# Optimization experiments

Hardware: AMD Instinct MI355X
Metric: run time of the kernel (lower is better)

The kernel has to match this reference:

```python
import jax, jax.numpy as jnp
import numpy as np

GROUPS = 32
EPS = 1e-6


def group_norm(x, gamma, beta):
    b, c, h, w = x.shape
    xg = x.reshape(b, GROUPS, c // GROUPS, h, w)
    mu = xg.mean(axis=(2, 3, 4), keepdims=True)
    var = xg.var(axis=(2, 3, 4), keepdims=True)
    xn = ((xg - mu) * jax.lax.rsqrt(var + EPS)).reshape(b, c, h, w)
    return xn * gamma[None, :, None, None] + beta[None, :, None, None]


def conv1x1(x, w, b):
    # x: (b,c_in,h,w), w: (c_out,c_in), b: (c_out,)
    return jnp.einsum('oc,bchw->bohw', w, x) + b[None, :, None, None]


def setup_inputs() -> dict:
    key = jax.random.key(0)
    ks = jax.random.split(key, 10)
    c = 512
    scale = 1.0 / np.sqrt(c)
    inp = jax.random.normal(ks[0], (16, c, 32, 32), dtype=jnp.float32)
    return {
        'inp': inp,
        'gamma': jnp.ones((c,), jnp.float32),
        'beta': jnp.zeros((c,), jnp.float32),
        'Wq': jax.random.normal(ks[1], (c, c), jnp.float32) * scale,
        'bq': jnp.zeros((c,), jnp.float32),
        'Wk': jax.random.normal(ks[2], (c, c), jnp.float32) * scale,
        'bk': jnp.zeros((c,), jnp.float32),
        'Wv': jax.random.normal(ks[3], (c, c), jnp.float32) * scale,
        'bv': jnp.zeros((c,), jnp.float32),
        'Wo': jax.random.normal(ks[4], (c, c), jnp.float32) * scale,
        'bo': jnp.zeros((c,), jnp.float32),
    }


def reference(inp, gamma, beta, Wq, bq, Wk, bk, Wv, bv, Wo, bo):
    b, c, h, w = inp.shape
    x = group_norm(inp, gamma, beta)
    Q = conv1x1(x, Wq, bq).reshape(b, c, h * w)  # (b,c,n)
    K = conv1x1(x, Wk, bk).reshape(b, c, h * w)  # (b,c,m)
    V = conv1x1(x, Wv, bv).reshape(b, c, h * w)  # (b,c,m)
    # attn[b,n,m] = sum_c Q[b,c,n] * K[b,c,m], scaled then softmax over m
    attn = jnp.einsum('bcn,bcm->bnm', Q, K) / jnp.sqrt(jnp.float32(c))
    attn = jax.nn.softmax(attn, axis=2)
    # A[b,c,n] = sum_m V[b,c,m] * attn[b,n,m]  (== bmm(V, attn^T))
    A = jnp.einsum('bcm,bnm->bcn', V, attn).reshape(b, c, h, w)
    A = conv1x1(A, Wo, bo)
    return inp + A
```

## Files before the change

kernel.cpp:

```cpp
#include <hip/hip_runtime.h>

typedef unsigned short UST;
typedef __attribute__((ext_vector_type(8))) short bf16x8;
typedef __attribute__((ext_vector_type(4))) float f32x4;

__device__ __forceinline__ UST f2bf(float f) {
  union { float f; unsigned int u; } x; x.f = f;
  unsigned int r = x.u + 0x7fffu + ((x.u >> 16) & 1u);
  return (UST)(r >> 16);
}

typedef const __attribute__((address_space(1))) unsigned int* gptr32;
typedef __attribute__((address_space(3))) unsigned int* lptr32;

__device__ __forceinline__ void load16(const void* g, void* l) {
  __builtin_amdgcn_global_load_lds((gptr32)(unsigned long long)g,
                                   (lptr32)(unsigned int)(unsigned long long)l,
                                   16, 0, 0);
}

__global__ __launch_bounds__(256) void conv_w(
    const float4* __restrict__ a, const float4* __restrict__ b,
    const float4* __restrict__ c, const float4* __restrict__ d,
    ushort4* __restrict__ oa, ushort4* __restrict__ ob,
    ushort4* __restrict__ oc, ushort4* __restrict__ od) {
  int i = blockIdx.x * 256 + threadIdx.x;
  float4 v;
  v = a[i]; oa[i] = make_ushort4(f2bf(v.x), f2bf(v.y), f2bf(v.z), f2bf(v.w));
  v = b[i]; ob[i] = make_ushort4(f2bf(v.x), f2bf(v.y), f2bf(v.z), f2bf(v.w));
  v = c[i]; oc[i] = make_ushort4(f2bf(v.x), f2bf(v.y), f2bf(v.z), f2bf(v.w));
  v = d[i]; od[i] = make_ushort4(f2bf(v.x), f2bf(v.y), f2bf(v.z), f2bf(v.w));
}

__global__ __launch_bounds__(256) void gn_stats(const float* __restrict__ inp,
                                                float* __restrict__ stats) {
  const int bg = blockIdx.x;
  const int tid = threadIdx.x;
  const float4* p = (const float4*)(inp + (size_t)bg * 16384);
  float s = 0.f, ss = 0.f;
#pragma unroll
  for (int i = 0; i < 16; i++) {
    float4 t = p[tid + i * 256];
    s += t.x + t.y + t.z + t.w;
    ss += t.x * t.x + t.y * t.y + t.z * t.z + t.w * t.w;
  }
  for (int o = 32; o >= 1; o >>= 1) { s += __shfl_xor(s, o); ss += __shfl_xor(ss, o); }
  __shared__ float red[8];
  const int w = tid >> 6;
  if ((tid & 63) == 0) { red[w * 2] = s; red[w * 2 + 1] = ss; }
  __syncthreads();
  if (tid == 0) {
    float S1 = red[0] + red[2] + red[4] + red[6];
    float S2 = red[1] + red[3] + red[5] + red[7];
    float mu = S1 * (1.f / 16384.f);
    float var = S2 * (1.f / 16384.f) - mu * mu;
    stats[bg * 2] = mu;
    stats[bg * 2 + 1] = rsqrtf(var + 1e-6f);
  }
}

__global__ __launch_bounds__(64) void gn_apply(
    const float* __restrict__ inp, const float* __restrict__ gamma,
    const float* __restrict__ beta, const float* __restrict__ stats,
    UST* __restrict__ Xnt) {
  const int lane = threadIdx.x;
  const int nc = blockIdx.x, g = blockIdx.y, b = blockIdx.z;
  const float mu = stats[(b * 32 + g) * 2];
  const float rstd = stats[(b * 32 + g) * 2 + 1];
  const int n = nc * 64 + lane;
  UST o[16];
#pragma unroll
  for (int j = 0; j < 16; j++) {
    int c = g * 16 + j;
    float sc = gamma[c] * rstd;
    float sh = beta[c] - mu * sc;
    float x = inp[((size_t)b * 512 + c) * 1024 + n];
    o[j] = f2bf(x * sc + sh);
  }
  UST* dst = Xnt + ((size_t)b * 1024 + n) * 512 + g * 16;
#pragma unroll
  for (int q = 0; q < 4; q++)
    ((ushort4*)dst)[q] = make_ushort4(o[q * 4], o[q * 4 + 1], o[q * 4 + 2], o[q * 4 + 3]);
}

__global__ __launch_bounds__(256) void softmax_k(const float* __restrict__ S,
                                                 UST* __restrict__ P) {
  const int w = threadIdx.x >> 6, lane = threadIdx.x & 63;
  const size_t row = (size_t)blockIdx.x * 4 + w;
  const float4* Sr = (const float4*)(S + row * 1024);
  float v[16];
#pragma unroll
  for (int j = 0; j < 4; j++) {
    float4 t = Sr[j * 64 + lane];
    v[j * 4 + 0] = t.x; v[j * 4 + 1] = t.y; v[j * 4 + 2] = t.z; v[j * 4 + 3] = t.w;
  }
  float m = v[0];
#pragma unroll
  for (int i = 1; i < 16; i++) m = fmaxf(m, v[i]);
#pragma unroll
  for (int o = 32; o >= 1; o >>= 1) m = fmaxf(m, __shfl_xor(m, o));
  float s = 0.f;
#pragma unroll
  for (int i = 0; i < 16; i++) { v[i] = __expf(v[i] - m); s += v[i]; }
#pragma unroll
  for (int o = 32; o >= 1; o >>= 1) s += __shfl_xor(s, o);
  const float rs = 1.f / s;
  ushort4* Pr = (ushort4*)(P + row * 1024);
#pragma unroll
  for (int j = 0; j < 4; j++)
    Pr[j * 64 + lane] = make_ushort4(f2bf(v[j * 4] * rs), f2bf(v[j * 4 + 1] * rs),
                                     f2bf(v[j * 4 + 2] * rs), f2bf(v[j * 4 + 3] * rs));
}

template <int EPI>
__global__ __launch_bounds__(256, 2) void gemm_bt(
    const UST* __restrict__ A, const UST* __restrict__ B, void* __restrict__ C,
    const float* __restrict__ bias, const float* __restrict__ extra, float scale,
    int M, int N, int K, long strideA, long strideB, long strideC) {
  __shared__ __align__(16) UST lA[128 * 32];
  __shared__ __align__(16) UST lB[128 * 32];

  const int tid = threadIdx.x;
  const int z = blockIdx.z;
  const int m0 = blockIdx.y * 128;
  const int n0 = blockIdx.x * 128;
  const UST* Ab = A + (long)z * strideA;
  const UST* Bb = B + (long)z * strideB;

  const int w = tid >> 6, lane = tid & 63;
  const int quad = lane >> 4, l16 = lane & 15;
  const int wm = w >> 1, wn = w & 1;

  f32x4 acc[4][4];
#pragma unroll
  for (int i = 0; i < 4; i++)
#pragma unroll
    for (int j = 0; j < 4; j++) acc[i][j] = f32x4{0.f, 0.f, 0.f, 0.f};

  const int rowa = tid >> 2;
  const int kc = (tid & 3) * 8;
  const UST* gA = Ab + (size_t)(m0 + rowa) * K + kc;
  const UST* gB = Bb + (size_t)(n0 + rowa) * K + kc;
  char* lAw = (char*)lA + (w << 10);
  char* lBw = (char*)lB + (w << 10);

  for (int k0 = 0; k0 < K; k0 += 32) {
    __syncthreads();
    load16(gA, lAw);
    load16(gA + (size_t)64 * K, lAw + 4096);
    load16(gB, lBw);
    load16(gB + (size_t)64 * K, lBw + 4096);
    gA += 32; gB += 32;
    __syncthreads();
    bf16x8 af[4], bfr[4];
#pragma unroll
    for (int i = 0; i < 4; i++)
      af[i] = *(const bf16x8*)(lA + (wm * 64 + i * 16 + l16) * 32 + quad * 8);
#pragma unroll
    for (int j = 0; j < 4; j++)
      bfr[j] = *(const bf16x8*)(lB + (wn * 64 + j * 16 + l16) * 32 + quad * 8);
#pragma unroll
    for (int i = 0; i < 4; i++)
#pragma unroll
      for (int j = 0; j < 4; j++)
        acc[i][j] = __builtin_amdgcn_mfma_f32_16x16x32_bf16(af[i], bfr[j], acc[i][j], 0, 0, 0);
  }

  const int gr0 = m0 + wm * 64 + quad * 4;
  const int gc0 = n0 + wn * 64 + l16;
  if constexpr (EPI == 2 || EPI == 4) {
    float* Cb = (float*)C + (long)z * strideC;
#pragma unroll
    for (int i = 0; i < 4; i++)
#pragma unroll
      for (int j = 0; j < 4; j++) {
        const int gc = gc0 + j * 16;
#pragma unroll
        for (int r = 0; r < 4; r++) {
          const int gr = gr0 + i * 16 + r;
          float v = acc[i][j][r];
          if constexpr (EPI == 2) v *= scale;
          if constexpr (EPI == 4) v += bias[gr] + extra[(long)z * strideC + (size_t)gr * N + gc];
          Cb[(size_t)gr * N + gc] = v;
        }
      }
  } else {
    UST* Cb = (UST*)C + (long)z * strideC;
#pragma unroll
    for (int i = 0; i < 4; i++)
#pragma unroll
      for (int j = 0; j < 4; j++) {
        const int gc = gc0 + j * 16;
        float bc = 0.f;
        if constexpr (EPI == 0) bc = bias[gc];
#pragma unroll
        for (int r = 0; r < 4; r++) {
          const int gr = gr0 + i * 16 + r;
          float v = acc[i][j][r] + bc;
          if constexpr (EPI == 1) v += bias[gr];
          Cb[(size_t)gr * N + gc] = f2bf(v);
        }
      }
  }
}

extern "C" void kernel_launch(void* const* d_in, const int* in_sizes, int n_in,
                              void* d_out, int out_size, void* d_ws, size_t ws_size,
                              hipStream_t stream) {
  const float* inp   = (const float*)d_in[0];
  const float* gamma = (const float*)d_in[1];
  const float* beta  = (const float*)d_in[2];
  const float* Wq    = (const float*)d_in[3];
  const float* bq    = (const float*)d_in[4];
  const float* Wk    = (const float*)d_in[5];
  const float* bk    = (const float*)d_in[6];
  const float* Wv    = (const float*)d_in[7];
  const float* bv    = (const float*)d_in[8];
  const float* Wo    = (const float*)d_in[9];
  const float* bo    = (const float*)d_in[10];
  float* out = (float*)d_out;
  char* ws = (char*)d_ws;

  UST*   Xnt   = (UST*)(ws);
  UST*   Qt    = (UST*)(ws + ((size_t)16 << 20));
  UST*   Kt    = (UST*)(ws + ((size_t)32 << 20));
  UST*   V     = (UST*)(ws + ((size_t)48 << 20));
  float* S     = (float*)(ws + ((size_t)64 << 20));
  float* stats = (float*)(ws + ((size_t)128 << 20));
  UST*   Wqb   = (UST*)(ws + ((size_t)128 << 20) + 8192);
  UST*   Wkb   = Wqb + 262144;
  UST*   Wvb   = Wkb + 262144;
  UST*   Wob   = Wvb + 262144;
  UST*   P     = Qt;
  UST*   At    = Xnt;

  conv_w<<<256, 256, 0, stream>>>((const float4*)Wq, (const float4*)Wk,
                                  (const float4*)Wv, (const float4*)Wo,
                                  (ushort4*)Wqb, (ushort4*)Wkb, (ushort4*)Wvb, (ushort4*)Wob);
  gn_stats<<<512, 256, 0, stream>>>(inp, stats);
  gn_apply<<<dim3(16, 32, 16), 64, 0, stream>>>(inp, gamma, beta, stats, Xnt);

  gemm_bt<0><<<dim3(4, 128, 1), 256, 0, stream>>>(Xnt, Wqb, Qt, bq, nullptr, 1.f,
                                                  16384, 512, 512, 0, 0, 0);
  gemm_bt<0><<<dim3(4, 128, 1), 256, 0, stream>>>(Xnt, Wkb, Kt, bk, nullptr, 1.f,
                                                  16384, 512, 512, 0, 0, 0);
  gemm_bt<1><<<dim3(8, 4, 16), 256, 0, stream>>>(Wvb, Xnt, V, bv, nullptr, 1.f,
                                                 512, 1024, 512, 0, 524288, 524288);
  gemm_bt<2><<<dim3(8, 8, 16), 256, 0, stream>>>(Qt, Kt, S, nullptr, nullptr,
                                                 0.04419417382415922f,
                                                 1024, 1024, 512, 524288, 524288, 1048576);
  softmax_k<<<4096, 256, 0, stream>>>(S, P);
  gemm_bt<3><<<dim3(4, 8, 16), 256, 0, stream>>>(P, V, At, nullptr, nullptr, 1.f,
                                                 1024, 512, 1024, 1048576, 524288, 524288);
  gemm_bt<4><<<dim3(8, 4, 16), 256, 0, stream>>>(Wob, At, out, bo, inp, 1.f,
                                                 512, 1024, 512, 0, 524288, 524288);
}
```

Measured before the change: 262.4 us.

## Fuse groupnorm passes, merge Q/K projections, store scores in bf16, blocked layout

Result: faster. 245.1 us (-6.6%).

```diff
diff --git a/kernel.cpp b/kernel.cpp
--- a/kernel.cpp
+++ b/kernel.cpp
@@ -2,6 +2,7 @@
 
 typedef unsigned short UST;
 typedef __attribute__((ext_vector_type(8))) short bf16x8;
+typedef __attribute__((ext_vector_type(8))) unsigned short us8;
 typedef __attribute__((ext_vector_type(4))) float f32x4;
 
 __device__ __forceinline__ UST f2bf(float f) {
@@ -9,6 +10,10 @@
   unsigned int r = x.u + 0x7fffu + ((x.u >> 16) & 1u);
   return (UST)(r >> 16);
 }
+__device__ __forceinline__ float bf2f(UST h) {
+  union { unsigned int u; float f; } x; x.u = ((unsigned int)h) << 16;
+  return x.f;
+}
 
 typedef const __attribute__((address_space(1))) unsigned int* gptr32;
 typedef __attribute__((address_space(3))) unsigned int* lptr32;
@@ -23,29 +28,38 @@
     const float4* __restrict__ a, const float4* __restrict__ b,
     const float4* __restrict__ c, const float4* __restrict__ d,
     ushort4* __restrict__ oa, ushort4* __restrict__ ob,
-    ushort4* __restrict__ oc, ushort4* __restrict__ od) {
+    ushort4* __restrict__ oc, ushort4* __restrict__ od,
+    const float4* __restrict__ bq4, const float4* __restrict__ bk4,
+    float4* __restrict__ bqk4) {
   int i = blockIdx.x * 256 + threadIdx.x;
   float4 v;
   v = a[i]; oa[i] = make_ushort4(f2bf(v.x), f2bf(v.y), f2bf(v.z), f2bf(v.w));
   v = b[i]; ob[i] = make_ushort4(f2bf(v.x), f2bf(v.y), f2bf(v.z), f2bf(v.w));
   v = c[i]; oc[i] = make_ushort4(f2bf(v.x), f2bf(v.y), f2bf(v.z), f2bf(v.w));
   v = d[i]; od[i] = make_ushort4(f2bf(v.x), f2bf(v.y), f2bf(v.z), f2bf(v.w));
-}
-
-__global__ __launch_bounds__(256) void gn_stats(const float* __restrict__ inp,
-                                                float* __restrict__ stats) {
-  const int bg = blockIdx.x;
+  if (blockIdx.x == 0) {
+    int t = threadIdx.x;
+    bqk4[t] = (t < 128) ? bq4[t] : bk4[t - 128];
+  }
+}
+
+__global__ __launch_bounds__(256) void gn_fused(
+    const float* __restrict__ inp, const float* __restrict__ gamma,
+    const float* __restrict__ beta, UST* __restrict__ Xnt) {
+  const int g = blockIdx.x & 31, b = blockIdx.x >> 5;
   const int tid = threadIdx.x;
-  const float4* p = (const float4*)(inp + (size_t)bg * 16384);
+  const float* base = inp + ((size_t)b * 32 + g) * 16384;
+  const float4* p4 = (const float4*)base;
   float s = 0.f, ss = 0.f;
 #pragma unroll
   for (int i = 0; i < 16; i++) {
-    float4 t = p[tid + i * 256];
+    float4 t = p4[tid + i * 256];
     s += t.x + t.y + t.z + t.w;
     ss += t.x * t.x + t.y * t.y + t.z * t.z + t.w * t.w;
   }
   for (int o = 32; o >= 1; o >>= 1) { s += __shfl_xor(s, o); ss += __shfl_xor(ss, o); }
   __shared__ float red[8];
+  __shared__ float mu_s, rstd_s;
   const int w = tid >> 6;
   if ((tid & 63) == 0) { red[w * 2] = s; red[w * 2 + 1] = ss; }
   __syncthreads();
@@ -54,46 +68,43 @@
     float S2 = red[1] + red[3] + red[5] + red[7];
     float mu = S1 * (1.f / 16384.f);
     float var = S2 * (1.f / 16384.f) - mu * mu;
-    stats[bg * 2] = mu;
-    stats[bg * 2 + 1] = rsqrtf(var + 1e-6f);
-  }
-}
-
-__global__ __launch_bounds__(64) void gn_apply(
-    const float* __restrict__ inp, const float* __restrict__ gamma,
-    const float* __restrict__ beta, const float* __restrict__ stats,
-    UST* __restrict__ Xnt) {
-  const int lane = threadIdx.x;
-  const int nc = blockIdx.x, g = blockIdx.y, b = blockIdx.z;
-  const float mu = stats[(b * 32 + g) * 2];
-  const float rstd = stats[(b * 32 + g) * 2 + 1];
-  const int n = nc * 64 + lane;
-  UST o[16];
-#pragma unroll
-  for (int j = 0; j < 16; j++) {
-    int c = g * 16 + j;
-    float sc = gamma[c] * rstd;
-    float sh = beta[c] - mu * sc;
-    float x = inp[((size_t)b * 512 + c) * 1024 + n];
-    o[j] = f2bf(x * sc + sh);
-  }
-  UST* dst = Xnt + ((size_t)b * 1024 + n) * 512 + g * 16;
-#pragma unroll
-  for (int q = 0; q < 4; q++)
-    ((ushort4*)dst)[q] = make_ushort4(o[q * 4], o[q * 4 + 1], o[q * 4 + 2], o[q * 4 + 3]);
-}
-
-__global__ __launch_bounds__(256) void softmax_k(const float* __restrict__ S,
+    mu_s = mu; rstd_s = rsqrtf(var + 1e-6f);
+  }
+  __syncthreads();
+  const float mu = mu_s, rstd = rstd_s;
+#pragma unroll
+  for (int cc = 0; cc < 2; cc++) {
+    const int ccg = g * 2 + cc;
+    float sc[8], sh[8];
+#pragma unroll
+    for (int j = 0; j < 8; j++) {
+      int ch = ccg * 8 + j;
+      sc[j] = gamma[ch] * rstd;
+      sh[j] = beta[ch] - mu * sc[j];
+    }
+#pragma unroll
+    for (int i = 0; i < 4; i++) {
+      const int n = tid + i * 256;
+      us8 v;
+#pragma unroll
+      for (int j = 0; j < 8; j++) {
+        float x = inp[((size_t)b * 512 + ccg * 8 + j) * 1024 + n];
+        v[j] = f2bf(x * sc[j] + sh[j]);
+      }
+      *(us8*)(Xnt + (size_t)b * 524288 + (size_t)ccg * 8192 + (size_t)n * 8) = v;
+    }
+  }
+}
+
+__global__ __launch_bounds__(256) void softmax_k(const UST* __restrict__ S,
                                                  UST* __restrict__ P) {
   const int w = threadIdx.x >> 6, lane = threadIdx.x & 63;
   const size_t row = (size_t)blockIdx.x * 4 + w;
-  const float4* Sr = (const float4*)(S + row * 1024);
+  const us8* Sr = (const us8*)(S + row * 1024);
+  us8 a = Sr[lane], b = Sr[64 + lane];
   float v[16];
 #pragma unroll
-  for (int j = 0; j < 4; j++) {
-    float4 t = Sr[j * 64 + lane];
-    v[j * 4 + 0] = t.x; v[j * 4 + 1] = t.y; v[j * 4 + 2] = t.z; v[j * 4 + 3] = t.w;
-  }
+  for (int j = 0; j < 8; j++) { v[j] = bf2f(a[j]); v[8 + j] = bf2f(b[j]); }
   float m = v[0];
 #pragma unroll
   for (int i = 1; i < 16; i++) m = fmaxf(m, v[i]);
@@ -105,18 +116,20 @@
 #pragma unroll
   for (int o = 32; o >= 1; o >>= 1) s += __shfl_xor(s, o);
   const float rs = 1.f / s;
-  ushort4* Pr = (ushort4*)(P + row * 1024);
-#pragma unroll
-  for (int j = 0; j < 4; j++)
-    Pr[j * 64 + lane] = make_ushort4(f2bf(v[j * 4] * rs), f2bf(v[j * 4 + 1] * rs),
-                                     f2bf(v[j * 4 + 2] * rs), f2bf(v[j * 4 + 3] * rs));
+  us8* Pr = (us8*)(P + row * 1024);
+  us8 oa, ob;
+#pragma unroll
+  for (int j = 0; j < 8; j++) { oa[j] = f2bf(v[j] * rs); ob[j] = f2bf(v[8 + j] * rs); }
+  Pr[lane] = oa; Pr[64 + lane] = ob;
 }
 
 template <int EPI>
 __global__ __launch_bounds__(256, 2) void gemm_bt(
     const UST* __restrict__ A, const UST* __restrict__ B, void* __restrict__ C,
     const float* __restrict__ bias, const float* __restrict__ extra, float scale,
-    int M, int N, int K, long strideA, long strideB, long strideC) {
+    int N, int K, int ldc,
+    int rsA, int csA, int ssA, int rsB, int csB, int ssB,
+    long zA, long zB, long zC) {
   __shared__ __align__(16) UST lA[128 * 32];
   __shared__ __align__(16) UST lB[128 * 32];
 
@@ -124,8 +137,8 @@
   const int z = blockIdx.z;
   const int m0 = blockIdx.y * 128;
   const int n0 = blockIdx.x * 128;
-  const UST* Ab = A + (long)z * strideA;
-  const UST* Bb = B + (long)z * strideB;
+  const UST* Ab = A + (long)z * zA;
+  const UST* Bb = B + (long)z * zB;
 
   const int w = tid >> 6, lane = tid & 63;
   const int quad = lane >> 4, l16 = lane & 15;
@@ -138,19 +151,19 @@
     for (int j = 0; j < 4; j++) acc[i][j] = f32x4{0.f, 0.f, 0.f, 0.f};
 
   const int rowa = tid >> 2;
-  const int kc = (tid & 3) * 8;
-  const UST* gA = Ab + (size_t)(m0 + rowa) * K + kc;
-  const UST* gB = Bb + (size_t)(n0 + rowa) * K + kc;
+  const int kchunk = tid & 3;
+  const UST* gA = Ab + (size_t)(m0 + rowa) * rsA + (size_t)kchunk * csA;
+  const UST* gB = Bb + (size_t)(n0 + rowa) * rsB + (size_t)kchunk * csB;
   char* lAw = (char*)lA + (w << 10);
   char* lBw = (char*)lB + (w << 10);
 
   for (int k0 = 0; k0 < K; k0 += 32) {
     __syncthreads();
     load16(gA, lAw);
-    load16(gA + (size_t)64 * K, lAw + 4096);
+    load16(gA + (size_t)64 * rsA, lAw + 4096);
     load16(gB, lBw);
-    load16(gB + (size_t)64 * K, lBw + 4096);
-    gA += 32; gB += 32;
+    load16(gB + (size_t)64 * rsB, lBw + 4096);
+    gA += ssA; gB += ssB;
     __syncthreads();
     bf16x8 af[4], bfr[4];
 #pragma unroll
@@ -168,8 +181,8 @@
 
   const int gr0 = m0 + wm * 64 + quad * 4;
   const int gc0 = n0 + wn * 64 + l16;
-  if constexpr (EPI == 2 || EPI == 4) {
-    float* Cb = (float*)C + (long)z * strideC;
+  if constexpr (EPI == 4) {
+    float* Cb = (float*)C + (long)z * zC;
 #pragma unroll
     for (int i = 0; i < 4; i++)
 #pragma unroll
@@ -178,14 +191,12 @@
 #pragma unroll
         for (int r = 0; r < 4; r++) {
           const int gr = gr0 + i * 16 + r;
-          float v = acc[i][j][r];
-          if constexpr (EPI == 2) v *= scale;
-          if constexpr (EPI == 4) v += bias[gr] + extra[(long)z * strideC + (size_t)gr * N + gc];
-          Cb[(size_t)gr * N + gc] = v;
+          float v = acc[i][j][r] + bias[gr] + extra[(long)z * zC + (size_t)gr * ldc + gc];
+          Cb[(size_t)gr * ldc + gc] = v;
         }
       }
   } else {
-    UST* Cb = (UST*)C + (long)z * strideC;
+    UST* Cb = (UST*)C + (long)z * zC;
 #pragma unroll
     for (int i = 0; i < 4; i++)
 #pragma unroll
@@ -198,7 +209,8 @@
           const int gr = gr0 + i * 16 + r;
           float v = acc[i][j][r] + bc;
           if constexpr (EPI == 1) v += bias[gr];
-          Cb[(size_t)gr * N + gc] = f2bf(v);
+          if constexpr (EPI == 5) v *= scale;
+          Cb[(size_t)gr * ldc + gc] = f2bf(v);
         }
       }
   }
@@ -221,37 +233,37 @@
   float* out = (float*)d_out;
   char* ws = (char*)d_ws;
 
-  UST*   Xnt   = (UST*)(ws);
-  UST*   Qt    = (UST*)(ws + ((size_t)16 << 20));
-  UST*   Kt    = (UST*)(ws + ((size_t)32 << 20));
-  UST*   V     = (UST*)(ws + ((size_t)48 << 20));
-  float* S     = (float*)(ws + ((size_t)64 << 20));
-  float* stats = (float*)(ws + ((size_t)128 << 20));
-  UST*   Wqb   = (UST*)(ws + ((size_t)128 << 20) + 8192);
-  UST*   Wkb   = Wqb + 262144;
-  UST*   Wvb   = Wkb + 262144;
-  UST*   Wob   = Wvb + 262144;
-  UST*   P     = Qt;
-  UST*   At    = Xnt;
-
-  conv_w<<<256, 256, 0, stream>>>((const float4*)Wq, (const float4*)Wk,
-                                  (const float4*)Wv, (const float4*)Wo,
-                                  (ushort4*)Wqb, (ushort4*)Wkb, (ushort4*)Wvb, (ushort4*)Wob);
-  gn_stats<<<512, 256, 0, stream>>>(inp, stats);
-  gn_apply<<<dim3(16, 32, 16), 64, 0, stream>>>(inp, gamma, beta, stats, Xnt);
-
-  gemm_bt<0><<<dim3(4, 128, 1), 256, 0, stream>>>(Xnt, Wqb, Qt, bq, nullptr, 1.f,
-                                                  16384, 512, 512, 0, 0, 0);
-  gemm_bt<0><<<dim3(4, 128, 1), 256, 0, stream>>>(Xnt, Wkb, Kt, bk, nullptr, 1.f,
-                                                  16384, 512, 512, 0, 0, 0);
-  gemm_bt<1><<<dim3(8, 4, 16), 256, 0, stream>>>(Wvb, Xnt, V, bv, nullptr, 1.f,
-                                                 512, 1024, 512, 0, 524288, 524288);
-  gemm_bt<2><<<dim3(8, 8, 16), 256, 0, stream>>>(Qt, Kt, S, nullptr, nullptr,
-                                                 0.04419417382415922f,
-                                                 1024, 1024, 512, 524288, 524288, 1048576);
+  UST*   Xnt  = (UST*)(ws);
+  UST*   QKt  = (UST*)(ws + ((size_t)16 << 20));
+  UST*   V    = (UST*)(ws + ((size_t)48 << 20));
+  UST*   S    = (UST*)(ws + ((size_t)64 << 20));
+  float* bqk  = (float*)(ws + ((size_t)96 << 20));
+  UST*   Wqkb = (UST*)(ws + ((size_t)96 << 20) + 8192);
+  UST*   Wvb  = Wqkb + 524288;
+  UST*   Wob  = Wvb + 262144;
+  UST*   P    = QKt;
+  UST*   At   = Xnt;
+
+  conv_w<<<256, 256, 0, stream>>>(
+      (const float4*)Wq, (const float4*)Wk, (const float4*)Wv, (const float4*)Wo,
+      (ushort4*)Wqkb, (ushort4*)(Wqkb + 262144), (ushort4*)Wvb, (ushort4*)Wob,
+      (const float4*)bq, (const float4*)bk, (float4*)bqk);
+  gn_fused<<<512, 256, 0, stream>>>(inp, gamma, beta, Xnt);
+
+  gemm_bt<0><<<dim3(8, 8, 16), 256, 0, stream>>>(
+      Xnt, Wqkb, QKt, bqk, nullptr, 1.f,
+      1024, 512, 1024, 8, 8192, 32768, 512, 8, 32, 524288, 0, 1048576);
+  gemm_bt<1><<<dim3(8, 4, 16), 256, 0, stream>>>(
+      Wvb, Xnt, V, bv, nullptr, 1.f,
+      1024, 512, 1024, 512, 8, 32, 8, 8192, 32768, 0, 524288, 524288);
+  gemm_bt<5><<<dim3(8, 8, 16), 256, 0, stream>>>(
+      QKt, QKt + 512, S, nullptr, nullptr, 0.04419417382415922f,
+      1024, 512, 1024, 1024, 8, 32, 1024, 8, 32, 1048576, 1048576, 1048576);
   softmax_k<<<4096, 256, 0, stream>>>(S, P);
-  gemm_bt<3><<<dim3(4, 8, 16), 256, 0, stream>>>(P, V, At, nullptr, nullptr, 1.f,
-                                                 1024, 512, 1024, 1048576, 524288, 524288);
-  gemm_bt<4><<<dim3(8, 4, 16), 256, 0, stream>>>(Wob, At, out, bo, inp, 1.f,
-                                                 512, 1024, 512, 0, 524288, 524288);
-}
+  gemm_bt<3><<<dim3(4, 8, 16), 256, 0, stream>>>(
+      P, V, At, nullptr, nullptr, 1.f,
+      512, 1024, 512, 1024, 8, 32, 1024, 8, 32, 1048576, 524288, 524288);
+  gemm_bt<4><<<dim3(8, 4, 16), 256, 0, stream>>>(
+      Wob, At, out, bo, inp, 1.f,
+      1024, 512, 1024, 512, 8, 32, 512, 8, 32, 0, 524288, 524288);
+}
```
